# Optimization experiments

Measured on AMD Instinct MI355X. Metric: run time of the kernel, lower is better.

The kernel has to match this reference:

```python
import jax, jax.numpy as jnp
import numpy as np

N = 25000   # nodes
E = 400000  # edges
F_IN = 128  # in_features
F_E = 16    # edge_features
C = 32      # channel_width
F_OUT = 1   # out_features
SLOPE = 0.01  # torch LeakyReLU default negative_slope


def leaky_relu(x):
    return jnp.where(x >= 0, x, SLOPE * x)


def setup_inputs() -> dict:
    key = jax.random.key(0)
    ks = jax.random.split(key, 12)
    x = jax.random.normal(ks[0], (N, F_IN), dtype=jnp.float32)
    edge_index = jax.random.randint(ks[1], (2, E), 0, N, dtype=jnp.int64)
    edge_attr = jax.random.normal(ks[2], (E, F_E), dtype=jnp.float32)
    # parameters (scaled like kaiming-ish fan-in init)
    W_in = jax.random.normal(ks[3], (F_IN, C), dtype=jnp.float32) / np.sqrt(F_IN)
    b_in = jnp.zeros((C,), dtype=jnp.float32)
    W_edge = jax.random.normal(ks[4], (F_E, C * C), dtype=jnp.float32) / np.sqrt(F_E)
    b_edge = jnp.zeros((C * C,), dtype=jnp.float32)
    W_root = jax.random.normal(ks[5], (C, C), dtype=jnp.float32) / np.sqrt(C)
    b_conv = jnp.zeros((C,), dtype=jnp.float32)
    W_out = jax.random.normal(ks[6], (C, F_OUT), dtype=jnp.float32) / np.sqrt(C)
    b_out = jnp.zeros((F_OUT,), dtype=jnp.float32)
    return {
        "x": x, "edge_index": edge_index, "edge_attr": edge_attr,
        "W_in": W_in, "b_in": b_in, "W_edge": W_edge, "b_edge": b_edge,
        "W_root": W_root, "b_conv": b_conv, "W_out": W_out, "b_out": b_out,
    }


def reference(x, edge_index, edge_attr, W_in, b_in, W_edge, b_edge,
              W_root, b_conv, W_out, b_out):
    # input projection (dropout = identity in eval mode)
    h = leaky_relu(x @ W_in + b_in)                       # [N, C]

    # NNConv layer (gnn_depth = 1):
    # per-edge weight matrix from edge_nn: Linear + LeakyReLU
    We = leaky_relu(edge_attr @ W_edge + b_edge)          # [E, C*C]
    We = We.reshape(E, C, C)                              # [E, C, C]
    src, dst = edge_index[0], edge_index[1]               # PyG: j=source, i=target
    # gather source node features, per-edge matvec, scatter-add to targets
    msg = jnp.einsum('ec,eco->eo', h[src], We)            # [E, C]
    aggr = jax.ops.segment_sum(msg, dst, num_segments=N)  # [N, C]
    h = aggr + h @ W_root + b_conv                        # root weight + bias
    h = leaky_relu(h)

    return h @ W_out + b_out                              # [N, F_OUT]
```

## Files before the change

kernel.cpp:

```cpp
#include <hip/hip_runtime.h>

#define NN 25000
#define EE 400000
#define FIN 128
#define FE 16
#define CH 32
#define SLOPE 0.01f
#define PROJ_BLOCKS 391
#define AUX_BLOCKS 32
#define WROW 24
#define WTP_SHORTS (1024 * WROW + 8)

typedef __attribute__((ext_vector_type(8))) short bf16x8;
typedef __attribute__((ext_vector_type(4))) float f32x4;

__device__ __forceinline__ float lrelu(float v) { return fmaxf(v, SLOPE * v); }

__device__ __forceinline__ f32x4 lrelu4(f32x4 v) {
    f32x4 s = v * SLOPE;
#if __has_builtin(__builtin_elementwise_max)
    return __builtin_elementwise_max(v, s);
#else
    f32x4 r;
    r[0] = fmaxf(v[0], s[0]); r[1] = fmaxf(v[1], s[1]);
    r[2] = fmaxf(v[2], s[2]); r[3] = fmaxf(v[3], s[3]);
    return r;
#endif
}

__device__ __forceinline__ short f2bf(float f) {
    union { float f; unsigned u; } v; v.f = f;
    unsigned r = (v.u + 0x7fffu + ((v.u >> 16) & 1u)) >> 16;
    return (short)r;
}

__global__ void __launch_bounds__(256)
k_pre(const float* __restrict__ x, const float* __restrict__ W_in,
      const float* __restrict__ b_in, const float* __restrict__ W_edge,
      const float* __restrict__ b_edge,
      float* __restrict__ h, float* __restrict__ aggr, short* __restrict__ WtP) {
    __shared__ short Wt1[CH * 136];
    int tid = threadIdx.x;

    if (blockIdx.x >= PROJ_BLOCKS) {
        int ab = blockIdx.x - PROJ_BLOCKS;
        if (ab < 4) {
            int co = ab * 256 + tid;
            short row[WROW] __attribute__((aligned(16)));
#pragma unroll
            for (int k = 0; k < 16; k++) row[k] = f2bf(W_edge[k * 1024 + co]);
            row[16] = f2bf(b_edge[co]);
#pragma unroll
            for (int k = 17; k < WROW; k++) row[k] = 0;
            uint4* dstp = (uint4*)(WtP + co * WROW);
            dstp[0] = ((uint4*)row)[0]; dstp[1] = ((uint4*)row)[1]; dstp[2] = ((uint4*)row)[2];
            if (ab == 0 && tid < 8) WtP[1024 * WROW + tid] = 0;
        } else {
            int t = (ab - 4) * 256 + tid;
            float4 z = make_float4(0.f, 0.f, 0.f, 0.f);
            for (int i = t; i < NN * CH / 4; i += (AUX_BLOCKS - 4) * 256)
                ((float4*)aggr)[i] = z;
        }
        return;
    }

#pragma unroll
    for (int i = 0; i < 16; i++) {
        int id = tid + 256 * i;
        int k = id >> 5, c = id & 31;
        Wt1[c * 136 + k] = f2bf(W_in[id]);
    }
    __syncthreads();

    int wave = tid >> 6, lane = tid & 63;
    int n16 = lane & 15, quad = lane >> 4;
    int node0 = blockIdx.x * 64 + wave * 16;

    f32x4 D[2];
#pragma unroll
    for (int ch = 0; ch < 2; ch++) {
        float bb = b_in[ch * 16 + n16];
        D[ch] = (f32x4){bb, bb, bb, bb};
    }
    int arow = node0 + n16; if (arow >= NN) arow = NN - 1;
#pragma unroll
    for (int kb = 0; kb < 4; kb++) {
        const float4* xp = (const float4*)(x + (size_t)arow * FIN + kb * 32 + quad * 8);
        float4 xa = xp[0], xb = xp[1];
        bf16x8 A = (bf16x8){f2bf(xa.x), f2bf(xa.y), f2bf(xa.z), f2bf(xa.w),
                            f2bf(xb.x), f2bf(xb.y), f2bf(xb.z), f2bf(xb.w)};
#pragma unroll
        for (int ch = 0; ch < 2; ch++) {
            bf16x8 B = *(const bf16x8*)&Wt1[(ch * 16 + n16) * 136 + kb * 32 + quad * 8];
            D[ch] = __builtin_amdgcn_mfma_f32_16x16x32_bf16(A, B, D[ch], 0, 0, 0);
        }
    }
#pragma unroll
    for (int ch = 0; ch < 2; ch++)
#pragma unroll
        for (int r = 0; r < 4; r++) {
            int nn = node0 + quad * 4 + r;
            if (nn < NN) h[(size_t)nn * CH + ch * 16 + n16] = lrelu(D[ch][r]);
        }
}

__global__ void __launch_bounds__(256, 2)
k_edge(const short* __restrict__ WtP,
       const float* __restrict__ ea,
       const int* __restrict__ src,
       const int* __restrict__ dst,
       const float* __restrict__ h,
       float* __restrict__ aggr) {
    __shared__ short WtL[WTP_SHORTS];
    __shared__ float hsT[CH * 132];

    int tid = threadIdx.x;
    int e0 = blockIdx.x * 128;

#pragma unroll
    for (int j = 0; j < 13; j++) {
        int idx = tid + 256 * j;
        if (idx < WTP_SHORTS / 8) ((uint4*)WtL)[idx] = ((const uint4*)WtP)[idx];
    }
    {
        int e = tid >> 1, half = tid & 1;
        int s = src[e0 + e];
        const float4* hp = (const float4*)(h + (size_t)s * CH + half * 16);
        float vv[16] __attribute__((aligned(16)));
        *(float4*)&vv[0] = hp[0]; *(float4*)&vv[4] = hp[1];
        *(float4*)&vv[8] = hp[2]; *(float4*)&vv[12] = hp[3];
#pragma unroll
        for (int j = 0; j < 16; j++) hsT[(half * 16 + j) * 132 + e] = vv[j];
    }
    __syncthreads();

    int wave = tid >> 6, lane = tid & 63;
    int n16 = lane & 15, quad = lane >> 4;
    int t0 = wave * 32, t1 = t0 + 16;

    bf16x8 A0 = (bf16x8){0,0,0,0,0,0,0,0}, A1 = A0;
    if (quad < 2) {
        const float4* p0 = (const float4*)(ea + (size_t)(e0 + t0 + n16) * FE + quad * 8);
        float4 a = p0[0], b = p0[1];
        A0 = (bf16x8){f2bf(a.x), f2bf(a.y), f2bf(a.z), f2bf(a.w),
                      f2bf(b.x), f2bf(b.y), f2bf(b.z), f2bf(b.w)};
        const float4* p1 = (const float4*)(ea + (size_t)(e0 + t1 + n16) * FE + quad * 8);
        a = p1[0]; b = p1[1];
        A1 = (bf16x8){f2bf(a.x), f2bf(a.y), f2bf(a.z), f2bf(a.w),
                      f2bf(b.x), f2bf(b.y), f2bf(b.z), f2bf(b.w)};
    } else if (quad == 2) {
        A0[0] = (short)0x3F80; A1[0] = (short)0x3F80;
    }

    f32x4 m0[2], m1[2];
    m0[0] = (f32x4){0,0,0,0}; m0[1] = m0[0]; m1[0] = m0[0]; m1[1] = m0[0];
    const f32x4 Z = (f32x4){0,0,0,0};

    const short* Bbase = WtL + n16 * WROW + quad * 8;
    const float* h0b = hsT + t0 + quad * 4;
    const float* h1b = hsT + t1 + quad * 4;

#pragma unroll
    for (int c4 = 0; c4 < 8; c4++) {
#pragma unroll
        for (int cc = 0; cc < 4; cc++) {
            int c = c4 * 4 + cc;
            f32x4 hc0 = *(const f32x4*)(h0b + c * 132);
            f32x4 hc1 = *(const f32x4*)(h1b + c * 132);
#pragma unroll
            for (int oh = 0; oh < 2; oh++) {
                int cb = c * 2 + oh;
                bf16x8 B = *(const bf16x8*)(Bbase + cb * (16 * WROW));
                f32x4 D0 = __builtin_amdgcn_mfma_f32_16x16x32_bf16(A0, B, Z, 0, 0, 0);
                f32x4 D1 = __builtin_amdgcn_mfma_f32_16x16x32_bf16(A1, B, Z, 0, 0, 0);
                m0[oh] += hc0 * lrelu4(D0);
                m1[oh] += hc1 * lrelu4(D1);
            }
        }
    }

#pragma unroll
    for (int r = 0; r < 4; r++) {
        int ed0 = dst[e0 + t0 + quad * 4 + r];
        int ed1 = dst[e0 + t1 + quad * 4 + r];
#pragma unroll
        for (int oh = 0; oh < 2; oh++) {
            unsafeAtomicAdd(&aggr[(size_t)ed0 * CH + oh * 16 + n16], m0[oh][r]);
            unsafeAtomicAdd(&aggr[(size_t)ed1 * CH + oh * 16 + n16], m1[oh][r]);
        }
    }
}

__global__ void __launch_bounds__(256)
k_node(const float* __restrict__ aggr,
       const float* __restrict__ h,
       const float* __restrict__ W_root,
       const float* __restrict__ b_conv,
       const float* __restrict__ W_out,
       const float* __restrict__ b_out,
       float* __restrict__ out) {
    __shared__ short WrB[CH * 40];
    __shared__ float WoS[CH];
    int tid = threadIdx.x;
    if (tid < 128) {
        int o = tid >> 2, c0 = (tid & 3) * 8;
        short tmp[8] __attribute__((aligned(16)));
#pragma unroll
        for (int j = 0; j < 8; j++) tmp[j] = f2bf(W_root[(c0 + j) * CH + o]);
        *(bf16x8*)&WrB[o * 40 + c0] = *(bf16x8*)tmp;
    } else if (tid < 160) {
        WoS[tid - 128] = W_out[tid - 128];
    }
    __syncthreads();

    int wave = tid >> 6, lane = tid & 63;
    int n16 = lane & 15, quad = lane >> 4;
    int node0 = blockIdx.x * 64 + wave * 16;

    int arow = node0 + n16; if (arow >= NN) arow = NN - 1;
    const float4* hp = (const float4*)(h + (size_t)arow * CH + quad * 8);
    float4 ha = hp[0], hb = hp[1];
    bf16x8 A = (bf16x8){f2bf(ha.x), f2bf(ha.y), f2bf(ha.z), f2bf(ha.w),
                        f2bf(hb.x), f2bf(hb.y), f2bf(hb.z), f2bf(hb.w)};
    float bc0 = b_conv[n16], bc1 = b_conv[16 + n16];
    f32x4 C0, C1;
#pragma unroll
    for (int r = 0; r < 4; r++) {
        int nr = node0 + quad * 4 + r; int cr = (nr < NN) ? nr : NN - 1;
        C0[r] = aggr[(size_t)cr * CH + n16] + bc0;
        C1[r] = aggr[(size_t)cr * CH + 16 + n16] + bc1;
    }
    bf16x8 B0 = *(const bf16x8*)&WrB[n16 * 40 + quad * 8];
    bf16x8 B1 = *(const bf16x8*)&WrB[(16 + n16) * 40 + quad * 8];
    f32x4 D0 = __builtin_amdgcn_mfma_f32_16x16x32_bf16(A, B0, C0, 0, 0, 0);
    f32x4 D1 = __builtin_amdgcn_mfma_f32_16x16x32_bf16(A, B1, C1, 0, 0, 0);

    float w0 = WoS[n16], w1 = WoS[16 + n16];
    f32x4 p;
#pragma unroll
    for (int r = 0; r < 4; r++)
        p[r] = lrelu(D0[r]) * w0 + lrelu(D1[r]) * w1;
#pragma unroll
    for (int mk = 1; mk < 16; mk <<= 1) {
#pragma unroll
        for (int r = 0; r < 4; r++) p[r] += __shfl_xor(p[r], mk, 64);
    }
    if (n16 == 0) {
        float bo = b_out[0];
#pragma unroll
        for (int r = 0; r < 4; r++) {
            int nr = node0 + quad * 4 + r;
            if (nr < NN) out[nr] = p[r] + bo;
        }
    }
}

extern "C" void kernel_launch(void* const* d_in, const int* in_sizes, int n_in,
                              void* d_out, int out_size, void* d_ws, size_t ws_size,
                              hipStream_t stream) {
    const float* x      = (const float*)d_in[0];
    const int*   ei     = (const int*)d_in[1];
    const float* ea     = (const float*)d_in[2];
    const float* W_in   = (const float*)d_in[3];
    const float* b_in   = (const float*)d_in[4];
    const float* W_edge = (const float*)d_in[5];
    const float* b_edge = (const float*)d_in[6];
    const float* W_root = (const float*)d_in[7];
    const float* b_conv = (const float*)d_in[8];
    const float* W_out  = (const float*)d_in[9];
    const float* b_out  = (const float*)d_in[10];
    float* out  = (float*)d_out;
    float* h    = (float*)d_ws;
    float* aggr = h + (size_t)NN * CH;
    short* WtP  = (short*)(aggr + (size_t)NN * CH);

    k_pre<<<PROJ_BLOCKS + AUX_BLOCKS, 256, 0, stream>>>(x, W_in, b_in, W_edge, b_edge,
                                                        h, aggr, WtP);
    k_edge<<<EE / 128, 256, 0, stream>>>(WtP, ea, ei, ei + EE, h, aggr);
    k_node<<<PROJ_BLOCKS, 256, 0, stream>>>(aggr, h, W_root, b_conv, W_out, b_out, out);
}
```

Before: 167.2 us.

## Store h and edge_attr as bf16 and process 256 edges per block

```diff
diff --git a/kernel.cpp b/kernel.cpp
--- a/kernel.cpp
+++ b/kernel.cpp
@@ -28,17 +28,18 @@
 #endif
 }
 
-__device__ __forceinline__ short f2bf(float f) {
+__device__ __forceinline__ unsigned short f2bf(float f) {
     union { float f; unsigned u; } v; v.f = f;
     unsigned r = (v.u + 0x7fffu + ((v.u >> 16) & 1u)) >> 16;
-    return (short)r;
+    return (unsigned short)r;
 }
 
 __global__ void __launch_bounds__(256)
 k_pre(const float* __restrict__ x, const float* __restrict__ W_in,
       const float* __restrict__ b_in, const float* __restrict__ W_edge,
-      const float* __restrict__ b_edge,
-      float* __restrict__ h, float* __restrict__ aggr, short* __restrict__ WtP) {
+      const float* __restrict__ b_edge, const float* __restrict__ ea,
+      unsigned short* __restrict__ h_bf, float* __restrict__ aggr,
+      short* __restrict__ WtP, short* __restrict__ ea_bf) {
     __shared__ short Wt1[CH * 136];
     int tid = threadIdx.x;
 
@@ -48,8 +49,8 @@
             int co = ab * 256 + tid;
             short row[WROW] __attribute__((aligned(16)));
 #pragma unroll
-            for (int k = 0; k < 16; k++) row[k] = f2bf(W_edge[k * 1024 + co]);
-            row[16] = f2bf(b_edge[co]);
+            for (int k = 0; k < 16; k++) row[k] = (short)f2bf(W_edge[k * 1024 + co]);
+            row[16] = (short)f2bf(b_edge[co]);
 #pragma unroll
             for (int k = 17; k < WROW; k++) row[k] = 0;
             uint4* dstp = (uint4*)(WtP + co * WROW);
@@ -60,6 +61,17 @@
             float4 z = make_float4(0.f, 0.f, 0.f, 0.f);
             for (int i = t; i < NN * CH / 4; i += (AUX_BLOCKS - 4) * 256)
                 ((float4*)aggr)[i] = z;
+            for (int e = t; e < EE; e += (AUX_BLOCKS - 4) * 256) {
+                const float4* p = (const float4*)(ea + (size_t)e * FE);
+                float4 a0 = p[0], a1 = p[1], a2 = p[2], a3 = p[3];
+                short rr[16] __attribute__((aligned(16)));
+                rr[0]=(short)f2bf(a0.x); rr[1]=(short)f2bf(a0.y); rr[2]=(short)f2bf(a0.z); rr[3]=(short)f2bf(a0.w);
+                rr[4]=(short)f2bf(a1.x); rr[5]=(short)f2bf(a1.y); rr[6]=(short)f2bf(a1.z); rr[7]=(short)f2bf(a1.w);
+                rr[8]=(short)f2bf(a2.x); rr[9]=(short)f2bf(a2.y); rr[10]=(short)f2bf(a2.z); rr[11]=(short)f2bf(a2.w);
+                rr[12]=(short)f2bf(a3.x); rr[13]=(short)f2bf(a3.y); rr[14]=(short)f2bf(a3.z); rr[15]=(short)f2bf(a3.w);
+                uint4* q = (uint4*)(ea_bf + (size_t)e * FE);
+                q[0] = ((uint4*)rr)[0]; q[1] = ((uint4*)rr)[1];
+            }
         }
         return;
     }
@@ -68,7 +80,7 @@
     for (int i = 0; i < 16; i++) {
         int id = tid + 256 * i;
         int k = id >> 5, c = id & 31;
-        Wt1[c * 136 + k] = f2bf(W_in[id]);
+        Wt1[c * 136 + k] = (short)f2bf(W_in[id]);
     }
     __syncthreads();
 
@@ -87,8 +99,8 @@
     for (int kb = 0; kb < 4; kb++) {
         const float4* xp = (const float4*)(x + (size_t)arow * FIN + kb * 32 + quad * 8);
         float4 xa = xp[0], xb = xp[1];
-        bf16x8 A = (bf16x8){f2bf(xa.x), f2bf(xa.y), f2bf(xa.z), f2bf(xa.w),
-                            f2bf(xb.x), f2bf(xb.y), f2bf(xb.z), f2bf(xb.w)};
+        bf16x8 A = (bf16x8){(short)f2bf(xa.x), (short)f2bf(xa.y), (short)f2bf(xa.z), (short)f2bf(xa.w),
+                            (short)f2bf(xb.x), (short)f2bf(xb.y), (short)f2bf(xb.z), (short)f2bf(xb.w)};
 #pragma unroll
         for (int ch = 0; ch < 2; ch++) {
             bf16x8 B = *(const bf16x8*)&Wt1[(ch * 16 + n16) * 136 + kb * 32 + quad * 8];
@@ -100,22 +112,22 @@
 #pragma unroll
         for (int r = 0; r < 4; r++) {
             int nn = node0 + quad * 4 + r;
-            if (nn < NN) h[(size_t)nn * CH + ch * 16 + n16] = lrelu(D[ch][r]);
+            if (nn < NN) h_bf[(size_t)nn * CH + ch * 16 + n16] = f2bf(lrelu(D[ch][r]));
         }
 }
 
 __global__ void __launch_bounds__(256, 2)
 k_edge(const short* __restrict__ WtP,
-       const float* __restrict__ ea,
+       const short* __restrict__ ea_bf,
        const int* __restrict__ src,
        const int* __restrict__ dst,
-       const float* __restrict__ h,
+       const unsigned short* __restrict__ h_bf,
        float* __restrict__ aggr) {
     __shared__ short WtL[WTP_SHORTS];
-    __shared__ float hsT[CH * 132];
+    __shared__ unsigned short hsB[CH * 264];
 
     int tid = threadIdx.x;
-    int e0 = blockIdx.x * 128;
+    int e0 = blockIdx.x * 256;
 
 #pragma unroll
     for (int j = 0; j < 13; j++) {
@@ -123,77 +135,86 @@
         if (idx < WTP_SHORTS / 8) ((uint4*)WtL)[idx] = ((const uint4*)WtP)[idx];
     }
     {
-        int e = tid >> 1, half = tid & 1;
-        int s = src[e0 + e];
-        const float4* hp = (const float4*)(h + (size_t)s * CH + half * 16);
-        float vv[16] __attribute__((aligned(16)));
-        *(float4*)&vv[0] = hp[0]; *(float4*)&vv[4] = hp[1];
-        *(float4*)&vv[8] = hp[2]; *(float4*)&vv[12] = hp[3];
-#pragma unroll
-        for (int j = 0; j < 16; j++) hsT[(half * 16 + j) * 132 + e] = vv[j];
+        int e = e0 + tid; if (e >= EE) e = EE - 1;
+        int s = src[e];
+        const uint4* hp = (const uint4*)(h_bf + (size_t)s * CH);
+        uint4 r0 = hp[0], r1 = hp[1], r2 = hp[2], r3 = hp[3];
+        unsigned w[8] = {r0.x, r0.y, r0.z, r0.w, r1.x, r1.y, r1.z, r1.w};
+        unsigned w2[8] = {r2.x, r2.y, r2.z, r2.w, r3.x, r3.y, r3.z, r3.w};
+#pragma unroll
+        for (int c2 = 0; c2 < 8; c2++) {
+            hsB[(2 * c2) * 264 + tid]     = (unsigned short)(w[c2] & 0xffffu);
+            hsB[(2 * c2 + 1) * 264 + tid] = (unsigned short)(w[c2] >> 16);
+            hsB[(16 + 2 * c2) * 264 + tid]     = (unsigned short)(w2[c2] & 0xffffu);
+            hsB[(16 + 2 * c2 + 1) * 264 + tid] = (unsigned short)(w2[c2] >> 16);
+        }
     }
     __syncthreads();
 
     int wave = tid >> 6, lane = tid & 63;
     int n16 = lane & 15, quad = lane >> 4;
-    int t0 = wave * 32, t1 = t0 + 16;
-
-    bf16x8 A0 = (bf16x8){0,0,0,0,0,0,0,0}, A1 = A0;
-    if (quad < 2) {
-        const float4* p0 = (const float4*)(ea + (size_t)(e0 + t0 + n16) * FE + quad * 8);
-        float4 a = p0[0], b = p0[1];
-        A0 = (bf16x8){f2bf(a.x), f2bf(a.y), f2bf(a.z), f2bf(a.w),
-                      f2bf(b.x), f2bf(b.y), f2bf(b.z), f2bf(b.w)};
-        const float4* p1 = (const float4*)(ea + (size_t)(e0 + t1 + n16) * FE + quad * 8);
-        a = p1[0]; b = p1[1];
-        A1 = (bf16x8){f2bf(a.x), f2bf(a.y), f2bf(a.z), f2bf(a.w),
-                      f2bf(b.x), f2bf(b.y), f2bf(b.z), f2bf(b.w)};
-    } else if (quad == 2) {
-        A0[0] = (short)0x3F80; A1[0] = (short)0x3F80;
-    }
-
-    f32x4 m0[2], m1[2];
-    m0[0] = (f32x4){0,0,0,0}; m0[1] = m0[0]; m1[0] = m0[0]; m1[1] = m0[0];
+    int ebase = e0 + wave * 64;
+    int lbase = wave * 64;
+
+    bf16x8 A[4];
+#pragma unroll
+    for (int t = 0; t < 4; t++) {
+        bf16x8 a = (bf16x8){0,0,0,0,0,0,0,0};
+        if (quad < 2) {
+            int e = ebase + t * 16 + n16; if (e >= EE) e = EE - 1;
+            a = *(const bf16x8*)(ea_bf + (size_t)e * FE + quad * 8);
+        } else if (quad == 2) {
+            a[0] = (short)0x3F80;
+        }
+        A[t] = a;
+    }
+
+    f32x4 m[4][2];
+#pragma unroll
+    for (int t = 0; t < 4; t++) { m[t][0] = (f32x4){0,0,0,0}; m[t][1] = m[t][0]; }
     const f32x4 Z = (f32x4){0,0,0,0};
 
-    const short* Bbase = WtL + n16 * WROW + quad * 8;
-    const float* h0b = hsT + t0 + quad * 4;
-    const float* h1b = hsT + t1 + quad * 4;
-
-#pragma unroll
-    for (int c4 = 0; c4 < 8; c4++) {
-#pragma unroll
-        for (int cc = 0; cc < 4; cc++) {
-            int c = c4 * 4 + cc;
-            f32x4 hc0 = *(const f32x4*)(h0b + c * 132);
-            f32x4 hc1 = *(const f32x4*)(h1b + c * 132);
-#pragma unroll
-            for (int oh = 0; oh < 2; oh++) {
-                int cb = c * 2 + oh;
-                bf16x8 B = *(const bf16x8*)(Bbase + cb * (16 * WROW));
-                f32x4 D0 = __builtin_amdgcn_mfma_f32_16x16x32_bf16(A0, B, Z, 0, 0, 0);
-                f32x4 D1 = __builtin_amdgcn_mfma_f32_16x16x32_bf16(A1, B, Z, 0, 0, 0);
-                m0[oh] += hc0 * lrelu4(D0);
-                m1[oh] += hc1 * lrelu4(D1);
+    const short* Bb = WtL + n16 * WROW + quad * 8;
+    const unsigned short* hb = hsB + lbase + quad * 4;
+
+#pragma unroll 4
+    for (int c = 0; c < 32; c++) {
+        f32x4 hf[4];
+#pragma unroll
+        for (int t = 0; t < 4; t++) {
+            uint2 raw = *(const uint2*)(hb + c * 264 + t * 16);
+            hf[t][0] = __uint_as_float(raw.x << 16);
+            hf[t][1] = __uint_as_float(raw.x & 0xffff0000u);
+            hf[t][2] = __uint_as_float(raw.y << 16);
+            hf[t][3] = __uint_as_float(raw.y & 0xffff0000u);
+        }
+#pragma unroll
+        for (int oh = 0; oh < 2; oh++) {
+            bf16x8 B = *(const bf16x8*)(Bb + (c * 2 + oh) * (16 * WROW));
+#pragma unroll
+            for (int t = 0; t < 4; t++) {
+                f32x4 D = __builtin_amdgcn_mfma_f32_16x16x32_bf16(A[t], B, Z, 0, 0, 0);
+                m[t][oh] += hf[t] * lrelu4(D);
             }
         }
     }
 
 #pragma unroll
-    for (int r = 0; r < 4; r++) {
-        int ed0 = dst[e0 + t0 + quad * 4 + r];
-        int ed1 = dst[e0 + t1 + quad * 4 + r];
-#pragma unroll
-        for (int oh = 0; oh < 2; oh++) {
-            unsafeAtomicAdd(&aggr[(size_t)ed0 * CH + oh * 16 + n16], m0[oh][r]);
-            unsafeAtomicAdd(&aggr[(size_t)ed1 * CH + oh * 16 + n16], m1[oh][r]);
-        }
-    }
+    for (int t = 0; t < 4; t++)
+#pragma unroll
+        for (int r = 0; r < 4; r++) {
+            int e = ebase + t * 16 + quad * 4 + r;
+            if (e < EE) {
+                int d = dst[e];
+                unsafeAtomicAdd(&aggr[(size_t)d * CH + n16],      m[t][0][r]);
+                unsafeAtomicAdd(&aggr[(size_t)d * CH + 16 + n16], m[t][1][r]);
+            }
+        }
 }
 
 __global__ void __launch_bounds__(256)
 k_node(const float* __restrict__ aggr,
-       const float* __restrict__ h,
+       const unsigned short* __restrict__ h_bf,
        const float* __restrict__ W_root,
        const float* __restrict__ b_conv,
        const float* __restrict__ W_out,
@@ -206,7 +227,7 @@
         int o = tid >> 2, c0 = (tid & 3) * 8;
         short tmp[8] __attribute__((aligned(16)));
 #pragma unroll
-        for (int j = 0; j < 8; j++) tmp[j] = f2bf(W_root[(c0 + j) * CH + o]);
+        for (int j = 0; j < 8; j++) tmp[j] = (short)f2bf(W_root[(c0 + j) * CH + o]);
         *(bf16x8*)&WrB[o * 40 + c0] = *(bf16x8*)tmp;
     } else if (tid < 160) {
         WoS[tid - 128] = W_out[tid - 128];
@@ -218,10 +239,7 @@
     int node0 = blockIdx.x * 64 + wave * 16;
 
     int arow = node0 + n16; if (arow >= NN) arow = NN - 1;
-    const float4* hp = (const float4*)(h + (size_t)arow * CH + quad * 8);
-    float4 ha = hp[0], hb = hp[1];
-    bf16x8 A = (bf16x8){f2bf(ha.x), f2bf(ha.y), f2bf(ha.z), f2bf(ha.w),
-                        f2bf(hb.x), f2bf(hb.y), f2bf(hb.z), f2bf(hb.w)};
+    bf16x8 A = *(const bf16x8*)(h_bf + (size_t)arow * CH + quad * 8);
     float bc0 = b_conv[n16], bc1 = b_conv[16 + n16];
     f32x4 C0, C1;
 #pragma unroll
@@ -269,13 +287,14 @@
     const float* b_conv = (const float*)d_in[8];
     const float* W_out  = (const float*)d_in[9];
     const float* b_out  = (const float*)d_in[10];
-    float* out  = (float*)d_out;
-    float* h    = (float*)d_ws;
-    float* aggr = h + (size_t)NN * CH;
-    short* WtP  = (short*)(aggr + (size_t)NN * CH);
+    float* out = (float*)d_out;
+    float* aggr = (float*)d_ws;
+    unsigned short* h_bf = (unsigned short*)(aggr + (size_t)NN * CH);
+    short* WtP  = (short*)(h_bf + (size_t)NN * CH);
+    short* ea_bf = WtP + WTP_SHORTS;
 
     k_pre<<<PROJ_BLOCKS + AUX_BLOCKS, 256, 0, stream>>>(x, W_in, b_in, W_edge, b_edge,
-                                                        h, aggr, WtP);
-    k_edge<<<EE / 128, 256, 0, stream>>>(WtP, ea, ei, ei + EE, h, aggr);
-    k_node<<<PROJ_BLOCKS, 256, 0, stream>>>(aggr, h, W_root, b_conv, W_out, b_out, out);
-}
+                                                        ea, h_bf, aggr, WtP, ea_bf);
+    k_edge<<<(EE + 255) / 256, 256, 0, stream>>>(WtP, ea_bf, ei, ei + EE, h_bf, aggr);
+    k_node<<<PROJ_BLOCKS, 256, 0, stream>>>(aggr, h_bf, W_root, b_conv, W_out, b_out, out);
+}
```

Result: slower. 288.7 us (+72.6%).

## Make edge kernel persistent with register prefetch of next tile

Applied to the files above, without the earlier changes.

```diff
diff --git a/kernel.cpp b/kernel.cpp
--- a/kernel.cpp
+++ b/kernel.cpp
@@ -7,7 +7,9 @@
 #define CH 32
 #define SLOPE 0.01f
 #define PROJ_BLOCKS 391
-#define AUX_BLOCKS 32
+#define AUX_BLOCKS 64
+#define NTILES 3125
+#define GRID_E 512
 #define WROW 24
 #define WTP_SHORTS (1024 * WROW + 8)
 
@@ -28,10 +30,10 @@
 #endif
 }
 
-__device__ __forceinline__ short f2bf(float f) {
+__device__ __forceinline__ unsigned short f2bf(float f) {
     union { float f; unsigned u; } v; v.f = f;
     unsigned r = (v.u + 0x7fffu + ((v.u >> 16) & 1u)) >> 16;
-    return (short)r;
+    return (unsigned short)r;
 }
 
 __global__ void __launch_bounds__(256)
@@ -48,12 +50,12 @@
             int co = ab * 256 + tid;
             short row[WROW] __attribute__((aligned(16)));
 #pragma unroll
-            for (int k = 0; k < 16; k++) row[k] = f2bf(W_edge[k * 1024 + co]);
-            row[16] = f2bf(b_edge[co]);
+            for (int k = 0; k < 16; k++) row[k] = (short)f2bf(W_edge[k * 1024 + co]);
+            row[16] = (short)f2bf(b_edge[co]);
 #pragma unroll
             for (int k = 17; k < WROW; k++) row[k] = 0;
-            uint4* dstp = (uint4*)(WtP + co * WROW);
-            dstp[0] = ((uint4*)row)[0]; dstp[1] = ((uint4*)row)[1]; dstp[2] = ((uint4*)row)[2];
+            uint4* dq = (uint4*)(WtP + co * WROW);
+            dq[0] = ((uint4*)row)[0]; dq[1] = ((uint4*)row)[1]; dq[2] = ((uint4*)row)[2];
             if (ab == 0 && tid < 8) WtP[1024 * WROW + tid] = 0;
         } else {
             int t = (ab - 4) * 256 + tid;
@@ -67,8 +69,7 @@
 #pragma unroll
     for (int i = 0; i < 16; i++) {
         int id = tid + 256 * i;
-        int k = id >> 5, c = id & 31;
-        Wt1[c * 136 + k] = f2bf(W_in[id]);
+        Wt1[(id & 31) * 136 + (id >> 5)] = (short)f2bf(W_in[id]);
     }
     __syncthreads();
 
@@ -87,8 +88,8 @@
     for (int kb = 0; kb < 4; kb++) {
         const float4* xp = (const float4*)(x + (size_t)arow * FIN + kb * 32 + quad * 8);
         float4 xa = xp[0], xb = xp[1];
-        bf16x8 A = (bf16x8){f2bf(xa.x), f2bf(xa.y), f2bf(xa.z), f2bf(xa.w),
-                            f2bf(xb.x), f2bf(xb.y), f2bf(xb.z), f2bf(xb.w)};
+        bf16x8 A = (bf16x8){(short)f2bf(xa.x), (short)f2bf(xa.y), (short)f2bf(xa.z), (short)f2bf(xa.w),
+                            (short)f2bf(xb.x), (short)f2bf(xb.y), (short)f2bf(xb.z), (short)f2bf(xb.w)};
 #pragma unroll
         for (int ch = 0; ch < 2; ch++) {
             bf16x8 B = *(const bf16x8*)&Wt1[(ch * 16 + n16) * 136 + kb * 32 + quad * 8];
@@ -115,78 +116,115 @@
     __shared__ float hsT[CH * 132];
 
     int tid = threadIdx.x;
-    int e0 = blockIdx.x * 128;
+    int wave = tid >> 6, lane = tid & 63;
+    int n16 = lane & 15, quad = lane >> 4;
+    int t0 = wave * 32, t1 = t0 + 16;
+    int eh = tid >> 1, half = tid & 1;
 
 #pragma unroll
     for (int j = 0; j < 13; j++) {
         int idx = tid + 256 * j;
         if (idx < WTP_SHORTS / 8) ((uint4*)WtL)[idx] = ((const uint4*)WtP)[idx];
     }
+
+    const short* Bb = WtL + n16 * WROW + quad * 8;
+    const float* h0b = hsT + t0 + quad * 4;
+    const float* h1b = hsT + t1 + quad * 4;
+    const f32x4 Z = (f32x4){0, 0, 0, 0};
+
+    float vv[16] __attribute__((aligned(16)));
+    bf16x8 An0, An1;
+    int dn0[4], dn1[4];
+
     {
-        int e = tid >> 1, half = tid & 1;
-        int s = src[e0 + e];
+        int e0 = blockIdx.x * 128;
+        int s = src[e0 + eh];
         const float4* hp = (const float4*)(h + (size_t)s * CH + half * 16);
-        float vv[16] __attribute__((aligned(16)));
         *(float4*)&vv[0] = hp[0]; *(float4*)&vv[4] = hp[1];
         *(float4*)&vv[8] = hp[2]; *(float4*)&vv[12] = hp[3];
-#pragma unroll
-        for (int j = 0; j < 16; j++) hsT[(half * 16 + j) * 132 + e] = vv[j];
-    }
-    __syncthreads();
-
-    int wave = tid >> 6, lane = tid & 63;
-    int n16 = lane & 15, quad = lane >> 4;
-    int t0 = wave * 32, t1 = t0 + 16;
-
-    bf16x8 A0 = (bf16x8){0,0,0,0,0,0,0,0}, A1 = A0;
-    if (quad < 2) {
-        const float4* p0 = (const float4*)(ea + (size_t)(e0 + t0 + n16) * FE + quad * 8);
-        float4 a = p0[0], b = p0[1];
-        A0 = (bf16x8){f2bf(a.x), f2bf(a.y), f2bf(a.z), f2bf(a.w),
-                      f2bf(b.x), f2bf(b.y), f2bf(b.z), f2bf(b.w)};
-        const float4* p1 = (const float4*)(ea + (size_t)(e0 + t1 + n16) * FE + quad * 8);
-        a = p1[0]; b = p1[1];
-        A1 = (bf16x8){f2bf(a.x), f2bf(a.y), f2bf(a.z), f2bf(a.w),
-                      f2bf(b.x), f2bf(b.y), f2bf(b.z), f2bf(b.w)};
-    } else if (quad == 2) {
-        A0[0] = (short)0x3F80; A1[0] = (short)0x3F80;
-    }
-
-    f32x4 m0[2], m1[2];
-    m0[0] = (f32x4){0,0,0,0}; m0[1] = m0[0]; m1[0] = m0[0]; m1[1] = m0[0];
-    const f32x4 Z = (f32x4){0,0,0,0};
-
-    const short* Bbase = WtL + n16 * WROW + quad * 8;
-    const float* h0b = hsT + t0 + quad * 4;
-    const float* h1b = hsT + t1 + quad * 4;
-
-#pragma unroll
-    for (int c4 = 0; c4 < 8; c4++) {
-#pragma unroll
-        for (int cc = 0; cc < 4; cc++) {
-            int c = c4 * 4 + cc;
-            f32x4 hc0 = *(const f32x4*)(h0b + c * 132);
-            f32x4 hc1 = *(const f32x4*)(h1b + c * 132);
+        An0 = (bf16x8){0,0,0,0,0,0,0,0}; An1 = An0;
+        if (quad < 2) {
+            const float4* p0 = (const float4*)(ea + (size_t)(e0 + t0 + n16) * FE + quad * 8);
+            float4 a = p0[0], b = p0[1];
+            An0 = (bf16x8){(short)f2bf(a.x), (short)f2bf(a.y), (short)f2bf(a.z), (short)f2bf(a.w),
+                           (short)f2bf(b.x), (short)f2bf(b.y), (short)f2bf(b.z), (short)f2bf(b.w)};
+            const float4* p1 = (const float4*)(ea + (size_t)(e0 + t1 + n16) * FE + quad * 8);
+            a = p1[0]; b = p1[1];
+            An1 = (bf16x8){(short)f2bf(a.x), (short)f2bf(a.y), (short)f2bf(a.z), (short)f2bf(a.w),
+                           (short)f2bf(b.x), (short)f2bf(b.y), (short)f2bf(b.z), (short)f2bf(b.w)};
+        } else if (quad == 2) {
+            An0[0] = (short)0x3F80; An1[0] = (short)0x3F80;
+        }
+#pragma unroll
+        for (int r = 0; r < 4; r++) {
+            dn0[r] = dst[e0 + t0 + quad * 4 + r];
+            dn1[r] = dst[e0 + t1 + quad * 4 + r];
+        }
+    }
+
+    for (int tile = blockIdx.x; tile < NTILES; tile += GRID_E) {
+        __syncthreads();
+#pragma unroll
+        for (int j = 0; j < 16; j++) hsT[(half * 16 + j) * 132 + eh] = vv[j];
+        __syncthreads();
+
+        bf16x8 A0 = An0, A1 = An1;
+        int dc0[4], dc1[4];
+#pragma unroll
+        for (int r = 0; r < 4; r++) { dc0[r] = dn0[r]; dc1[r] = dn1[r]; }
+
+        int ntile = tile + GRID_E;
+        if (ntile < NTILES) {
+            int e0 = ntile * 128;
+            int s = src[e0 + eh];
+            const float4* hp = (const float4*)(h + (size_t)s * CH + half * 16);
+            *(float4*)&vv[0] = hp[0]; *(float4*)&vv[4] = hp[1];
+            *(float4*)&vv[8] = hp[2]; *(float4*)&vv[12] = hp[3];
+            if (quad < 2) {
+                const float4* p0 = (const float4*)(ea + (size_t)(e0 + t0 + n16) * FE + quad * 8);
+                float4 a = p0[0], b = p0[1];
+                An0 = (bf16x8){(short)f2bf(a.x), (short)f2bf(a.y), (short)f2bf(a.z), (short)f2bf(a.w),
+                               (short)f2bf(b.x), (short)f2bf(b.y), (short)f2bf(b.z), (short)f2bf(b.w)};
+                const float4* p1 = (const float4*)(ea + (size_t)(e0 + t1 + n16) * FE + quad * 8);
+                a = p1[0]; b = p1[1];
+                An1 = (bf16x8){(short)f2bf(a.x), (short)f2bf(a.y), (short)f2bf(a.z), (short)f2bf(a.w),
+                               (short)f2bf(b.x), (short)f2bf(b.y), (short)f2bf(b.z), (short)f2bf(b.w)};
+            }
+#pragma unroll
+            for (int r = 0; r < 4; r++) {
+                dn0[r] = dst[e0 + t0 + quad * 4 + r];
+                dn1[r] = dst[e0 + t1 + quad * 4 + r];
+            }
+        }
+
+        f32x4 m0[2], m1[2];
+        m0[0] = Z; m0[1] = Z; m1[0] = Z; m1[1] = Z;
+#pragma unroll
+        for (int c4 = 0; c4 < 8; c4++) {
+#pragma unroll
+            for (int cc = 0; cc < 4; cc++) {
+                int c = c4 * 4 + cc;
+                f32x4 hc0 = *(const f32x4*)(h0b + c * 132);
+                f32x4 hc1 = *(const f32x4*)(h1b + c * 132);
+#pragma unroll
+                for (int oh = 0; oh < 2; oh++) {
+                    int cb = c * 2 + oh;
+                    bf16x8 B = *(const bf16x8*)(Bb + cb * (16 * WROW));
+                    f32x4 D0 = __builtin_amdgcn_mfma_f32_16x16x32_bf16(A0, B, Z, 0, 0, 0);
+                    f32x4 D1 = __builtin_amdgcn_mfma_f32_16x16x32_bf16(A1, B, Z, 0, 0, 0);
+                    m0[oh] += hc0 * lrelu4(D0);
+                    m1[oh] += hc1 * lrelu4(D1);
+                }
+            }
+        }
+
+#pragma unroll
+        for (int r = 0; r < 4; r++) {
 #pragma unroll
             for (int oh = 0; oh < 2; oh++) {
-                int cb = c * 2 + oh;
-                bf16x8 B = *(const bf16x8*)(Bbase + cb * (16 * WROW));
-                f32x4 D0 = __builtin_amdgcn_mfma_f32_16x16x32_bf16(A0, B, Z, 0, 0, 0);
-                f32x4 D1 = __builtin_amdgcn_mfma_f32_16x16x32_bf16(A1, B, Z, 0, 0, 0);
-                m0[oh] += hc0 * lrelu4(D0);
-                m1[oh] += hc1 * lrelu4(D1);
+                unsafeAtomicAdd(&aggr[(size_t)dc0[r] * CH + oh * 16 + n16], m0[oh][r]);
+                unsafeAtomicAdd(&aggr[(size_t)dc1[r] * CH + oh * 16 + n16], m1[oh][r]);
             }
-        }
-    }
-
-#pragma unroll
-    for (int r = 0; r < 4; r++) {
-        int ed0 = dst[e0 + t0 + quad * 4 + r];
-        int ed1 = dst[e0 + t1 + quad * 4 + r];
-#pragma unroll
-        for (int oh = 0; oh < 2; oh++) {
-            unsafeAtomicAdd(&aggr[(size_t)ed0 * CH + oh * 16 + n16], m0[oh][r]);
-            unsafeAtomicAdd(&aggr[(size_t)ed1 * CH + oh * 16 + n16], m1[oh][r]);
         }
     }
 }
@@ -206,7 +244,7 @@
         int o = tid >> 2, c0 = (tid & 3) * 8;
         short tmp[8] __attribute__((aligned(16)));
 #pragma unroll
-        for (int j = 0; j < 8; j++) tmp[j] = f2bf(W_root[(c0 + j) * CH + o]);
+        for (int j = 0; j < 8; j++) tmp[j] = (short)f2bf(W_root[(c0 + j) * CH + o]);
         *(bf16x8*)&WrB[o * 40 + c0] = *(bf16x8*)tmp;
     } else if (tid < 160) {
         WoS[tid - 128] = W_out[tid - 128];
@@ -220,8 +258,8 @@
     int arow = node0 + n16; if (arow >= NN) arow = NN - 1;
     const float4* hp = (const float4*)(h + (size_t)arow * CH + quad * 8);
     float4 ha = hp[0], hb = hp[1];
-    bf16x8 A = (bf16x8){f2bf(ha.x), f2bf(ha.y), f2bf(ha.z), f2bf(ha.w),
-                        f2bf(hb.x), f2bf(hb.y), f2bf(hb.z), f2bf(hb.w)};
+    bf16x8 A = (bf16x8){(short)f2bf(ha.x), (short)f2bf(ha.y), (short)f2bf(ha.z), (short)f2bf(ha.w),
+                        (short)f2bf(hb.x), (short)f2bf(hb.y), (short)f2bf(hb.z), (short)f2bf(hb.w)};
     float bc0 = b_conv[n16], bc1 = b_conv[16 + n16];
     f32x4 C0, C1;
 #pragma unroll
@@ -276,6 +314,6 @@
 
     k_pre<<<PROJ_BLOCKS + AUX_BLOCKS, 256, 0, stream>>>(x, W_in, b_in, W_edge, b_edge,
                                                         h, aggr, WtP);
-    k_edge<<<EE / 128, 256, 0, stream>>>(WtP, ea, ei, ei + EE, h, aggr);
+    k_edge<<<GRID_E, 256, 0, stream>>>(WtP, ea, ei, ei + EE, h, aggr);
     k_node<<<PROJ_BLOCKS, 256, 0, stream>>>(aggr, h, W_root, b_conv, W_out, b_out, out);
 }
```

Result: no change. 170.1 us (+1.7%).
